# Kernel optimization log

Hardware: AMD Instinct MI355X
Metric: run time of the kernel (lower is better)

The kernel has to match this reference:

```python
import jax, jax.numpy as jnp
import numpy as np

A, B, D, L = 256, 64, 768, 2  # annotators, batch, hidden, num_labels
G1, G2 = 4, 8                 # groups per attribute


def setup_inputs() -> dict:
    key = jax.random.key(0)
    ks = jax.random.split(key, 9)
    s = 1.0 / np.sqrt(D)
    return {
        "pooled": jax.random.normal(ks[0], (B, D), jnp.float32),
        "W1": jax.random.normal(ks[1], (G1, D, D), jnp.float32) * s,
        "b1": jax.random.normal(ks[2], (G1, D), jnp.float32) * s,
        "W2": jax.random.normal(ks[3], (G2, D, D), jnp.float32) * s,
        "b2": jax.random.normal(ks[4], (G2, D), jnp.float32) * s,
        "Wh": jax.random.normal(ks[5], (A, D, L), jnp.float32) * s,
        "bh": jax.random.normal(ks[6], (A, L), jnp.float32) * s,
        "g1_idx": jax.random.randint(ks[7], (A,), 0, G1),
        "g2_idx": jax.random.randint(ks[8], (A,), 0, G2),
    }


def reference(pooled, W1, b1, W2, b2, Wh, bh, g1_idx, g2_idx):
    # Attribute 1: every annotator with the same group shares the transform,
    # so compute once per group then gather (avoids A redundant GEMMs).
    h_g = jnp.einsum('bd,gde->gbe', pooled, W1) + b1[:, None, :]   # [G1, B, D]
    h = h_g[g1_idx]                                                # [A, B, D]
    # Attribute 2: input now differs per annotator -> grouped GEMM via gathered weights.
    h = jnp.einsum('abd,ade->abe', h, W2[g2_idx]) + b2[g2_idx][:, None, :]  # [A, B, D]
    # Per-annotator classification heads.
    logits = jnp.einsum('abd,adl->abl', h, Wh) + bh[:, None, :]    # [A, B, L]
    # Match torch layout: logits[batch, annotator, label]
    return jnp.transpose(logits, (1, 0, 2))                        # [B, A, L]
```

## Files before the change

kernel.cpp:

```cpp
#include <hip/hip_runtime.h>

#define AN 256
#define BN 64
#define DN 768
#define LN 2
#define G1N 4
#define G2N 8
#define KI (DN / 32)
#define PAD 776

typedef __attribute__((ext_vector_type(8))) short short8;
typedef __attribute__((ext_vector_type(4))) short bf16x4;
typedef __attribute__((ext_vector_type(4))) float floatx4;

static __device__ __forceinline__ unsigned short f2bf(float f) {
    union { float f; unsigned int u; } v; v.f = f;
    unsigned int r = v.u + 0x7FFF + ((v.u >> 16) & 1);
    return (unsigned short)(r >> 16);
}
static __device__ __forceinline__ unsigned int pack2(float a, float b) {
    return (unsigned int)f2bf(a) | ((unsigned int)f2bf(b) << 16);
}

__global__ __launch_bounds__(256) void k_main(
    const float* __restrict__ pooled, const float* __restrict__ W1,
    const float* __restrict__ b1, const float* __restrict__ W2,
    const float* __restrict__ b2, const float* __restrict__ Wh,
    const float* __restrict__ bh, const int* __restrict__ g2i,
    unsigned short* __restrict__ h1, unsigned short* __restrict__ Wcs,
    float* __restrict__ bc)
{
    __shared__ __align__(16) unsigned char smem[26880];
    const int tid = threadIdx.x, bx = blockIdx.x;
    const int lane = tid & 63, wave = tid >> 6;
    const int nn = lane & 15, quad = lane >> 4;

    if (bx < 192) {
        float* ldsW = (float*)smem;
        const int g = bx / 48, e0 = (bx % 48) * 16;
        const float* src = W1 + (size_t)g * DN * DN + e0;
        const int r = tid >> 3, c2 = (tid & 7) * 2;

        {
            float2 v = *(const float2*)(src + (size_t)r * DN + c2);
            float* d = ldsW + r * 17 + c2;
            d[0] = v.x; d[1] = v.y;
        }
        __syncthreads();

        const int mt = wave;
        const float* Ap = pooled + (size_t)(mt * 16 + nn) * DN + quad * 8;
        floatx4 acc = {0, 0, 0, 0};
        for (int kk = 0; kk < KI; ++kk) {
            const int cur = kk & 1;
            float2 vnext;
            if (kk + 1 < KI)
                vnext = *(const float2*)(src + (size_t)((kk + 1) * 32 + r) * DN + c2);

            const float* wb = ldsW + cur * 544 + quad * 8 * 17 + nn;
            short8 bf;
            #pragma unroll
            for (int j = 0; j < 8; ++j)
                bf[j] = (short)f2bf(wb[j * 17]);

            float4 a0 = *(const float4*)(Ap + kk * 32);
            float4 a1 = *(const float4*)(Ap + kk * 32 + 4);
            short8 af;
            af[0] = (short)f2bf(a0.x); af[1] = (short)f2bf(a0.y);
            af[2] = (short)f2bf(a0.z); af[3] = (short)f2bf(a0.w);
            af[4] = (short)f2bf(a1.x); af[5] = (short)f2bf(a1.y);
            af[6] = (short)f2bf(a1.z); af[7] = (short)f2bf(a1.w);

            acc = __builtin_amdgcn_mfma_f32_16x16x32_bf16(af, bf, acc, 0, 0, 0);

            if (kk + 1 < KI) {
                float* d = ldsW + (cur ^ 1) * 544 + r * 17 + c2;
                d[0] = vnext.x; d[1] = vnext.y;
            }
            __syncthreads();
        }

        const int e = e0 + nn;
        const float bv = b1[g * DN + e];
        #pragma unroll
        for (int rr = 0; rr < 4; ++rr)
            h1[(size_t)g * BN * DN + (size_t)(mt * 16 + quad * 4 + rr) * DN + e] =
                f2bf(acc[rr] + bv);
    } else if (bx < 288) {
        int* g2s  = (int*)smem;
        int* lst2 = (int*)(smem + 1024);
        unsigned short* Whs = (unsigned short*)(smem + 2048);

        const int j = bx - 192, g = j / 12, mbase = (j % 12) * 64;

        const int m_row = mbase + wave * 16 + nn;
        const float* ap = W2 + ((size_t)g * DN + m_row) * DN + quad * 8;
        short8 Areg[KI];
        #pragma unroll
        for (int kk = 0; kk < KI; ++kk) {
            float4 a0 = *(const float4*)(ap + kk * 32);
            float4 a1 = *(const float4*)(ap + kk * 32 + 4);
            short8 af;
            af[0] = (short)f2bf(a0.x); af[1] = (short)f2bf(a0.y);
            af[2] = (short)f2bf(a0.z); af[3] = (short)f2bf(a0.w);
            af[4] = (short)f2bf(a1.x); af[5] = (short)f2bf(a1.y);
            af[6] = (short)f2bf(a1.z); af[7] = (short)f2bf(a1.w);
            Areg[kk] = af;
        }

        g2s[tid] = g2i[tid];
        __syncthreads();
        const int my = g2s[tid];
        int rk = 0;
        for (int a2 = 0; a2 < tid; ++a2) rk += (g2s[a2] == my);
        if (my == g) lst2[rk] = tid;
        int n2g = 0;
        for (int a2 = 0; a2 < AN; ++a2) n2g += (g2s[a2] == g);
        __syncthreads();
        const int cols = 2 * n2g;

        const int al = tid >> 5, t32 = tid & 31;
        for (int c0 = 0; c0 < cols; c0 += 16) {
            const int sidx = (c0 >> 1) + al;
            if (sidx < n2g) {
                const int a = lst2[sidx];
                const float4* wa4 = (const float4*)(Wh + (size_t)a * (DN * LN));
                #pragma unroll
                for (int i = 0; i < 12; ++i) {
                    const int f4 = i * 32 + t32;
                    float4 v = wa4[f4];
                    const int e2 = f4 * 2;
                    *(unsigned int*)(Whs + (2 * al)     * PAD + e2) = pack2(v.x, v.z);
                    *(unsigned int*)(Whs + (2 * al + 1) * PAD + e2) = pack2(v.y, v.w);
                }
            }
            __syncthreads();
            const unsigned short* Brow = Whs + nn * PAD + quad * 8;
            floatx4 acc = {0, 0, 0, 0};
            #pragma unroll
            for (int kk = 0; kk < KI; ++kk) {
                short8 bf = *(const short8*)(Brow + kk * 32);
                acc = __builtin_amdgcn_mfma_f32_16x16x32_bf16(Areg[kk], bf, acc, 0, 0, 0);
            }
            const int c = c0 + nn;
            if (c < cols) {
                const int dbase = mbase + wave * 16 + quad * 4;
                bf16x4 v;
                #pragma unroll
                for (int rr = 0; rr < 4; ++rr) v[rr] = (short)f2bf(acc[rr]);
                *(bf16x4*)(Wcs + (size_t)(g * 256 + c) * DN + dbase) = v;
            }
            __syncthreads();
        }
    } else {
        const int jb = bx - 288;
        const int aa = tid >> 3, jj = tid & 7;
        const int a = jb * 32 + aa;
        const int gv2 = g2i[a];
        const float* whp = Wh + (size_t)a * (DN * LN);
        const float* b2p = b2 + gv2 * DN;
        float acc0 = 0.f, acc1 = 0.f;
        #pragma unroll 4
        for (int i = 0; i < 48; ++i) {
            int e = jj * 96 + i * 2;
            float4 w4 = *(const float4*)(whp + e * 2);
            float2 bv = *(const float2*)(b2p + e);
            acc0 += bv.x * w4.x + bv.y * w4.z;
            acc1 += bv.x * w4.y + bv.y * w4.w;
        }
        #pragma unroll
        for (int off = 4; off; off >>= 1) {
            acc0 += __shfl_down(acc0, off, 64);
            acc1 += __shfl_down(acc1, off, 64);
        }
        if (jj == 0) {
            bc[a * 2 + 0] = acc0 + bh[a * 2 + 0];
            bc[a * 2 + 1] = acc1 + bh[a * 2 + 1];
        }
    }
}

__global__ __launch_bounds__(256) void k_out(
    const unsigned short* __restrict__ h1, const unsigned short* __restrict__ Wcs,
    const float* __restrict__ bc, const int* __restrict__ g1i,
    const int* __restrict__ g2i, float* __restrict__ out)
{
    __shared__ int g1s[AN], g2s[AN], lst1[AN], sx2[AN];
    const int g = blockIdx.y;
    const int tid = threadIdx.x;
    g1s[tid] = g1i[tid];
    g2s[tid] = g2i[tid];
    __syncthreads();
    const int m1 = g1s[tid], m2 = g2s[tid];
    int r1 = 0, r2 = 0;
    for (int a2 = 0; a2 < tid; ++a2) {
        r1 += (g1s[a2] == m1);
        r2 += (g2s[a2] == m2);
    }
    sx2[tid] = r2;
    if (m1 == g) lst1[r1] = tid;
    int n1g = 0;
    for (int a2 = 0; a2 < AN; ++a2) n1g += (g1s[a2] == g);
    __syncthreads();

    const int cols = 2 * n1g;
    const int nt0 = blockIdx.x * 16;
    if (nt0 >= cols) return;

    const int lane = tid & 63, wave = tid >> 6;
    const int nn = lane & 15, quad = lane >> 4;

    const int c = nt0 + nn;
    const bool valid = (c < cols);
    const int cl = valid ? c : (cols - 1);
    const int a = lst1[cl >> 1];
    const int l = cl & 1;
    const int rp = (g2s[a] * 128 + sx2[a]) * 2 + l;

    const unsigned short* hg = h1 + (size_t)g * BN * DN + (size_t)(wave * 16 + nn) * DN + quad * 8;
    const unsigned short* wp = Wcs + (size_t)rp * DN + quad * 8;

    floatx4 acc = {0, 0, 0, 0};
    #pragma unroll
    for (int kk = 0; kk < KI; ++kk) {
        short8 af = *(const short8*)(hg + kk * 32);
        short8 bf = *(const short8*)(wp + kk * 32);
        acc = __builtin_amdgcn_mfma_f32_16x16x32_bf16(af, bf, acc, 0, 0, 0);
    }
    if (valid) {
        const float bv = bc[a * 2 + l];
        #pragma unroll
        for (int r = 0; r < 4; ++r)
            out[(size_t)(wave * 16 + quad * 4 + r) * (AN * LN) + a * 2 + l] = acc[r] + bv;
    }
}

extern "C" void kernel_launch(void* const* d_in, const int* in_sizes, int n_in,
                              void* d_out, int out_size, void* d_ws, size_t ws_size,
                              hipStream_t stream) {
    const float* pooled = (const float*)d_in[0];
    const float* W1     = (const float*)d_in[1];
    const float* b1     = (const float*)d_in[2];
    const float* W2     = (const float*)d_in[3];
    const float* b2     = (const float*)d_in[4];
    const float* Wh     = (const float*)d_in[5];
    const float* bh     = (const float*)d_in[6];
    const int*   g1i    = (const int*)d_in[7];
    const int*   g2i    = (const int*)d_in[8];
    float* out = (float*)d_out;

    char* ws = (char*)d_ws;
    float* bc = (float*)ws;                           ws += 512 * 4;
    unsigned short* h1  = (unsigned short*)ws;        ws += (size_t)G1N * BN * DN * 2;
    unsigned short* Wcs = (unsigned short*)ws;

    dim3 blk(256);
    k_main<<<dim3(296),   blk, 0, stream>>>(pooled, W1, b1, W2, b2, Wh, bh, g2i,
                                            h1, Wcs, bc);
    k_out <<<dim3(32, 4), blk, 0, stream>>>(h1, Wcs, bc, g1i, g2i, out);
}
```

Before: 131.2 us.

## Stage full W1 column tile as bf16 in LDS, widen blocks to 32 columns

The attribute-1 GEMM blocks now load a whole 768x32 slab of W1 into LDS at once, converted to bf16 and transposed. The old design streamed 32-row chunks through a double-buffered fp32 LDS tile with a barrier on every k-step. Each block now computes two 16-column MFMA tiles, which halves the number of W1 blocks and removes the per-iteration synchronisation and repeated conversion. The costs are a larger LDS footprint, fewer blocks in flight for this stage, and a transposed LDS write pattern that may cause bank conflicts.

```diff
diff --git a/kernel.cpp b/kernel.cpp
--- a/kernel.cpp
+++ b/kernel.cpp
@@ -30,39 +30,33 @@
     unsigned short* __restrict__ h1, unsigned short* __restrict__ Wcs,
     float* __restrict__ bc)
 {
-    __shared__ __align__(16) unsigned char smem[26880];
+    __shared__ __align__(16) unsigned char smem[49664];
     const int tid = threadIdx.x, bx = blockIdx.x;
     const int lane = tid & 63, wave = tid >> 6;
     const int nn = lane & 15, quad = lane >> 4;
 
-    if (bx < 192) {
-        float* ldsW = (float*)smem;
-        const int g = bx / 48, e0 = (bx % 48) * 16;
+    if (bx < 96) {
+        unsigned short* Wt = (unsigned short*)smem;
+        const int g = bx / 24, e0 = (bx % 24) * 32;
         const float* src = W1 + (size_t)g * DN * DN + e0;
-        const int r = tid >> 3, c2 = (tid & 7) * 2;
-
-        {
-            float2 v = *(const float2*)(src + (size_t)r * DN + c2);
-            float* d = ldsW + r * 17 + c2;
-            d[0] = v.x; d[1] = v.y;
+        const int dr = tid >> 3, q8 = tid & 7;
+
+        #pragma unroll
+        for (int round = 0; round < 24; ++round) {
+            const int d = round * 32 + dr;
+            float4 v = *(const float4*)(src + (size_t)d * DN + q8 * 4);
+            Wt[(q8 * 4 + 0) * PAD + d] = f2bf(v.x);
+            Wt[(q8 * 4 + 1) * PAD + d] = f2bf(v.y);
+            Wt[(q8 * 4 + 2) * PAD + d] = f2bf(v.z);
+            Wt[(q8 * 4 + 3) * PAD + d] = f2bf(v.w);
         }
         __syncthreads();
 
         const int mt = wave;
         const float* Ap = pooled + (size_t)(mt * 16 + nn) * DN + quad * 8;
-        floatx4 acc = {0, 0, 0, 0};
+        floatx4 acc0 = {0, 0, 0, 0}, acc1 = {0, 0, 0, 0};
+        #pragma unroll
         for (int kk = 0; kk < KI; ++kk) {
-            const int cur = kk & 1;
-            float2 vnext;
-            if (kk + 1 < KI)
-                vnext = *(const float2*)(src + (size_t)((kk + 1) * 32 + r) * DN + c2);
-
-            const float* wb = ldsW + cur * 544 + quad * 8 * 17 + nn;
-            short8 bf;
-            #pragma unroll
-            for (int j = 0; j < 8; ++j)
-                bf[j] = (short)f2bf(wb[j * 17]);
-
             float4 a0 = *(const float4*)(Ap + kk * 32);
             float4 a1 = *(const float4*)(Ap + kk * 32 + 4);
             short8 af;
@@ -70,28 +64,27 @@
             af[2] = (short)f2bf(a0.z); af[3] = (short)f2bf(a0.w);
             af[4] = (short)f2bf(a1.x); af[5] = (short)f2bf(a1.y);
             af[6] = (short)f2bf(a1.z); af[7] = (short)f2bf(a1.w);
-
-            acc = __builtin_amdgcn_mfma_f32_16x16x32_bf16(af, bf, acc, 0, 0, 0);
-
-            if (kk + 1 < KI) {
-                float* d = ldsW + (cur ^ 1) * 544 + r * 17 + c2;
-                d[0] = vnext.x; d[1] = vnext.y;
-            }
-            __syncthreads();
-        }
-
-        const int e = e0 + nn;
-        const float bv = b1[g * DN + e];
-        #pragma unroll
-        for (int rr = 0; rr < 4; ++rr)
-            h1[(size_t)g * BN * DN + (size_t)(mt * 16 + quad * 4 + rr) * DN + e] =
-                f2bf(acc[rr] + bv);
-    } else if (bx < 288) {
+            short8 bf0 = *(const short8*)(Wt + (size_t)nn * PAD + kk * 32 + quad * 8);
+            short8 bf1 = *(const short8*)(Wt + (size_t)(16 + nn) * PAD + kk * 32 + quad * 8);
+            acc0 = __builtin_amdgcn_mfma_f32_16x16x32_bf16(af, bf0, acc0, 0, 0, 0);
+            acc1 = __builtin_amdgcn_mfma_f32_16x16x32_bf16(af, bf1, acc1, 0, 0, 0);
+        }
+
+        const float bv0 = b1[g * DN + e0 + nn];
+        const float bv1 = b1[g * DN + e0 + 16 + nn];
+        unsigned short* hrow = h1 + (size_t)g * BN * DN;
+        #pragma unroll
+        for (int rr = 0; rr < 4; ++rr) {
+            const size_t ro = (size_t)(mt * 16 + quad * 4 + rr) * DN;
+            hrow[ro + e0 + nn]      = f2bf(acc0[rr] + bv0);
+            hrow[ro + e0 + 16 + nn] = f2bf(acc1[rr] + bv1);
+        }
+    } else if (bx < 192) {
         int* g2s  = (int*)smem;
         int* lst2 = (int*)(smem + 1024);
         unsigned short* Whs = (unsigned short*)(smem + 2048);
 
-        const int j = bx - 192, g = j / 12, mbase = (j % 12) * 64;
+        const int j = bx - 96, g = j / 12, mbase = (j % 12) * 64;
 
         const int m_row = mbase + wave * 16 + nn;
         const float* ap = W2 + ((size_t)g * DN + m_row) * DN + quad * 8;
@@ -153,7 +146,7 @@
             __syncthreads();
         }
     } else {
-        const int jb = bx - 288;
+        const int jb = bx - 192;
         const int aa = tid >> 3, jj = tid & 7;
         const int a = jb * 32 + aa;
         const int gv2 = g2i[a];
@@ -255,7 +248,7 @@
     unsigned short* Wcs = (unsigned short*)ws;
 
     dim3 blk(256);
-    k_main<<<dim3(296),   blk, 0, stream>>>(pooled, W1, b1, W2, b2, Wh, bh, g2i,
+    k_main<<<dim3(200),   blk, 0, stream>>>(pooled, W1, b1, W2, b2, Wh, bh, g2i,
                                             h1, Wcs, bc);
     k_out <<<dim3(32, 4), blk, 0, stream>>>(h1, Wcs, bc, g1i, g2i, out);
 }
```

Result: faster. 117.8 us (-10.2%).
